# Kernel tuning notes

Hardware: AMD Instinct MI355X
Metric: run time of the kernel (lower is better)

The kernel has to match this reference:

```python
import jax, jax.numpy as jnp
import numpy as np

CAPACITY_FACTOR = 1.25


def setup_inputs() -> dict:
    key = jax.random.key(0)
    k1, k2, k3, k4 = jax.random.split(key, 4)
    B, T, H = 2, 2048, 1024
    E, F = 8, 2048
    x = jax.random.normal(k1, (B, T, H), dtype=jnp.float32)
    Wr = jax.random.normal(k2, (H, E), dtype=jnp.float32) * 0.02
    W1 = jax.random.normal(k3, (E, H, 2 * F), dtype=jnp.float32) * 0.02
    W2 = jax.random.normal(k4, (E, F, H), dtype=jnp.float32) * 0.02
    return {"x": x, "Wr": Wr, "W1": W1, "W2": W2}


def _moe_forward(x, Wr, W1, W2):
    B, T, H = x.shape
    E = Wr.shape[1]
    N = B * T
    cap = max(1, int(CAPACITY_FACTOR * (N * 2 / E)))  # static (shape-derived)

    flat_x = x.reshape(N, H)
    logits = flat_x @ Wr                      # [N, E] (train=False: no noise)
    gate = jax.nn.softmax(logits, axis=-1)
    top2_val, top2_idx = jax.lax.top_k(gate, 2)   # [N,2]

    # --- capacity bookkeeping, matching the torch sequential fill order ---
    e0, e1 = top2_idx[:, 0], top2_idx[:, 1]
    oh0 = jax.nn.one_hot(e0, E, dtype=jnp.int32)  # [N,E]
    oh1 = jax.nn.one_hot(e1, E, dtype=jnp.int32)
    # rank of each token within its expert's k=0 queue (flattened token order)
    pos0 = jnp.take_along_axis(jnp.cumsum(oh0, axis=0), top2_idx[:, :1], axis=1)[:, 0] - 1
    count0 = oh0.sum(axis=0)                      # tokens routed top-1 per expert
    used0 = jnp.minimum(count0, cap)              # slots consumed in k=0 pass
    keep0 = pos0 < cap
    # k=1 pass starts after the slots used by k=0
    pos1 = jnp.take_along_axis(jnp.cumsum(oh1, axis=0), top2_idx[:, 1:2], axis=1)[:, 0] - 1
    pos1 = pos1 + used0[e1]
    keep1 = pos1 < cap

    dummy = E * cap  # drop slot
    slot0 = jnp.where(keep0, e0 * cap + pos0, dummy)
    slot1 = jnp.where(keep1, e1 * cap + pos1, dummy)

    # --- dispatch: [E*cap+1, H] buffer (last row is the drop slot) ---
    buf = jnp.zeros((E * cap + 1, H), dtype=x.dtype)
    buf = buf.at[slot0].set(flat_x).at[slot1].set(flat_x)
    xe = buf[: E * cap].reshape(E, cap, H)

    # --- grouped expert FFN (SwiGLU) ---
    h = jnp.einsum("ech,ehf->ecf", xe, W1)        # [E, cap, 2F]
    a, b = jnp.split(h, 2, axis=-1)
    act = jax.nn.silu(a) * b                      # [E, cap, F]
    out = jnp.einsum("ecf,efh->ech", act, W2)     # [E, cap, H]
    out_flat = out.reshape(E * cap, H)

    # --- combine: gather back per token, weighted by gate values ---
    g0 = out_flat[jnp.where(keep0, slot0, 0)] * keep0[:, None]
    g1 = out_flat[jnp.where(keep1, slot1, 0)] * keep1[:, None]
    y = g0 * top2_val[:, 0:1] + g1 * top2_val[:, 1:2]
    y = y.reshape(B, T, H)

    # --- balance loss ---
    me = 1e-9
    prob_per_expert = gate.mean(axis=0)                 # == mean over (B,T)
    used1 = (oh1 * keep1[:, None].astype(jnp.int32)).sum(axis=0)
    used = (used0 + used1).astype(gate.dtype)
    frac_used = jnp.maximum(used, me) / (N * 2 + me)
    balance_loss = (prob_per_expert * frac_used).sum() * E
    return y, balance_loss


def reference(x, Wr, W1, W2):
    return _moe_forward(x, Wr, W1, W2)
```

## Files before the change

### kernel.cpp

```cpp
#include <hip/hip_runtime.h>
#include <cstdint>

#define E_    8
#define H_    1024
#define F_    2048
#define NTOK  4096
#define CAP   1280
#define ECAP  (E_*CAP)

typedef unsigned short u16;
typedef __attribute__((ext_vector_type(8))) short bf16x8;
typedef __attribute__((ext_vector_type(4))) float f32x4;
typedef __attribute__((ext_vector_type(4))) unsigned short u16x4;

__device__ __forceinline__ u16 f2bf(float f) {
  union { float f; uint32_t u; } v; v.f = f;
  uint32_t r = v.u + 0x7fffu + ((v.u >> 16) & 1u);
  return (u16)(r >> 16);
}

__device__ __forceinline__ void gld16(const void* gsrc, void* ldst) {
  auto g = reinterpret_cast<const __attribute__((address_space(1))) uint32_t*>(
      reinterpret_cast<uintptr_t>(gsrc));
  auto l = reinterpret_cast<__attribute__((address_space(3))) uint32_t*>(
      reinterpret_cast<uintptr_t>(ldst));
  __builtin_amdgcn_global_load_lds(g, l, 16, 0, 0);
}

__device__ __forceinline__ int swz(int row, int chunk) {
  return row * 64 + ((chunk ^ (row & 7)) * 8);
}

__global__ __launch_bounds__(256) void transpose_cvt(const float* __restrict__ in,
                                                     u16* __restrict__ outp,
                                                     int R, int C) {
  __shared__ float tile[64][65];
  size_t base = (size_t)blockIdx.z * R * C;
  int r0 = blockIdx.y * 64, c0 = blockIdx.x * 64;
  int tx = threadIdx.x, ty = threadIdx.y;
#pragma unroll
  for (int i = 0; i < 4; i++) {
    int row = ty + 16 * i;
    float4 v = *(const float4*)(in + base + (size_t)(r0 + row) * C + c0 + tx * 4);
    tile[row][tx * 4 + 0] = v.x;
    tile[row][tx * 4 + 1] = v.y;
    tile[row][tx * 4 + 2] = v.z;
    tile[row][tx * 4 + 3] = v.w;
  }
  __syncthreads();
#pragma unroll
  for (int i = 0; i < 4; i++) {
    int c = ty + 16 * i;
    u16x4 b;
    b.x = f2bf(tile[tx * 4 + 0][c]);
    b.y = f2bf(tile[tx * 4 + 1][c]);
    b.z = f2bf(tile[tx * 4 + 2][c]);
    b.w = f2bf(tile[tx * 4 + 3][c]);
    *(u16x4*)(outp + base + (size_t)(c0 + c) * R + r0 + tx * 4) = b;
  }
}

__global__ __launch_bounds__(256) void router_kernel(const float* __restrict__ x,
                                                     const float* __restrict__ Wr,
                                                     int* __restrict__ e0o, int* __restrict__ e1o,
                                                     float* __restrict__ v0o, float* __restrict__ v1o,
                                                     float* __restrict__ partial) {
  int w = threadIdx.x >> 6, l = threadIdx.x & 63;
  int t = blockIdx.x * 4 + w;
  const float* xr = x + (size_t)t * H_;
  float acc[8] = {0.f,0.f,0.f,0.f,0.f,0.f,0.f,0.f};
#pragma unroll
  for (int it = 0; it < 16; ++it) {
    int h = it * 64 + l;
    float xv = xr[h];
    const float4* wr = (const float4*)(Wr + h * 8);
    float4 wa = wr[0], wb = wr[1];
    acc[0] += xv * wa.x; acc[1] += xv * wa.y; acc[2] += xv * wa.z; acc[3] += xv * wa.w;
    acc[4] += xv * wb.x; acc[5] += xv * wb.y; acc[6] += xv * wb.z; acc[7] += xv * wb.w;
  }
#pragma unroll
  for (int e = 0; e < 8; ++e)
#pragma unroll
    for (int off = 32; off; off >>= 1)
      acc[e] += __shfl_xor(acc[e], off);

  __shared__ float pg[4][8];
  if (l == 0) {
    float mx = acc[0];
#pragma unroll
    for (int e = 1; e < 8; ++e) mx = fmaxf(mx, acc[e]);
    float g[8], s = 0.f;
#pragma unroll
    for (int e = 0; e < 8; ++e) { g[e] = __expf(acc[e] - mx); s += g[e]; }
    float inv = 1.f / s;
#pragma unroll
    for (int e = 0; e < 8; ++e) g[e] *= inv;
    int b0 = 0; float m0 = g[0];
#pragma unroll
    for (int e = 1; e < 8; ++e) if (g[e] > m0) { m0 = g[e]; b0 = e; }
    int b1 = -1; float m1 = -1.f;
#pragma unroll
    for (int e = 0; e < 8; ++e) if (e != b0 && g[e] > m1) { m1 = g[e]; b1 = e; }
    e0o[t] = b0; e1o[t] = b1; v0o[t] = m0; v1o[t] = m1;
#pragma unroll
    for (int e = 0; e < 8; ++e) pg[w][e] = g[e];
  }
  __syncthreads();
  if (threadIdx.x < 8) {
    int e = threadIdx.x;
    partial[blockIdx.x * 8 + e] = pg[0][e] + pg[1][e] + pg[2][e] + pg[3][e];
  }
}

__global__ __launch_bounds__(256) void scan_kernel(const int* __restrict__ e0i, const int* __restrict__ e1i,
                                                   const float* __restrict__ partial,
                                                   int* __restrict__ slot0, int* __restrict__ slot1,
                                                   float* __restrict__ bl_out) {
  __shared__ int c0[256][8], c1[256][8];
  __shared__ float gs[256][8];
  __shared__ int used0_s[8], tot1_s[8];
  int tid = threadIdx.x;

  int le0[16], le1[16];
  int lc0[8] = {0,0,0,0,0,0,0,0}, lc1[8] = {0,0,0,0,0,0,0,0};
  for (int i = 0; i < 16; ++i) {
    int t = tid * 16 + i;
    le0[i] = e0i[t]; le1[i] = e1i[t];
    lc0[le0[i]]++; lc1[le1[i]]++;
  }
#pragma unroll
  for (int e = 0; e < 8; ++e) { c0[tid][e] = lc0[e]; c1[tid][e] = lc1[e]; }

  float g[8] = {0.f,0.f,0.f,0.f,0.f,0.f,0.f,0.f};
  for (int rr = 0; rr < 4; ++rr)
#pragma unroll
    for (int e = 0; e < 8; ++e) g[e] += partial[(tid + rr * 256) * 8 + e];
#pragma unroll
  for (int e = 0; e < 8; ++e) gs[tid][e] = g[e];
  __syncthreads();

  for (int d = 1; d < 256; d <<= 1) {
    int t0[8], t1[8];
    bool a = (tid >= d);
    if (a) {
#pragma unroll
      for (int e = 0; e < 8; ++e) { t0[e] = c0[tid - d][e]; t1[e] = c1[tid - d][e]; }
    }
    __syncthreads();
    if (a) {
#pragma unroll
      for (int e = 0; e < 8; ++e) { c0[tid][e] += t0[e]; c1[tid][e] += t1[e]; }
    }
    __syncthreads();
  }
  for (int s = 128; s > 0; s >>= 1) {
    if (tid < s)
#pragma unroll
      for (int e = 0; e < 8; ++e) gs[tid][e] += gs[tid + s][e];
    __syncthreads();
  }
  if (tid < 8) {
    int e = tid;
    used0_s[e] = min(c0[255][e], CAP);
    tot1_s[e] = c1[255][e];
  }
  __syncthreads();

  int ex0[8], ex1[8];
#pragma unroll
  for (int e = 0; e < 8; ++e) { ex0[e] = c0[tid][e] - lc0[e]; ex1[e] = c1[tid][e] - lc1[e]; }
  int r0c[8] = {0,0,0,0,0,0,0,0}, r1c[8] = {0,0,0,0,0,0,0,0};
  for (int i = 0; i < 16; ++i) {
    int t = tid * 16 + i;
    int e = le0[i];
    int pos = ex0[e] + r0c[e]; r0c[e]++;
    slot0[t] = (pos < CAP) ? (e * CAP + pos) : -1;
    e = le1[i];
    pos = ex1[e] + r1c[e] + used0_s[e]; r1c[e]++;
    slot1[t] = (pos < CAP) ? (e * CAP + pos) : -1;
  }

  if (tid == 0) {
    float bl = 0.f;
    for (int e = 0; e < 8; ++e) {
      int u1 = min(tot1_s[e], max(0, CAP - used0_s[e]));
      float used = (float)(used0_s[e] + u1);
      float fu = fmaxf(used, 1e-9f) / (8192.f + 1e-9f);
      bl += (gs[0][e] / (float)NTOK) * fu;
    }
    bl_out[0] = bl * 8.f;
  }
}

__global__ __launch_bounds__(256) void scatter_kernel(const float* __restrict__ x,
                                                      const int* __restrict__ slot0,
                                                      const int* __restrict__ slot1,
                                                      u16* __restrict__ xe) {
  int t = blockIdx.x, tid = threadIdx.x;
  float4 vv = *(const float4*)(x + (size_t)t * H_ + tid * 4);
  u16x4 b;
  b.x = f2bf(vv.x); b.y = f2bf(vv.y); b.z = f2bf(vv.z); b.w = f2bf(vv.w);
  int s0 = slot0[t], s1 = slot1[t];
  if (s0 >= 0) *(u16x4*)(xe + (size_t)s0 * H_ + tid * 4) = b;
  if (s1 >= 0) *(u16x4*)(xe + (size_t)s1 * H_ + tid * 4) = b;
}

__global__ __launch_bounds__(512, 2) void gemm1_kernel(const u16* __restrict__ xe,
                                                       const u16* __restrict__ W1T,
                                                       u16* __restrict__ act) {
  __shared__ u16 As[2][256 * 64];
  __shared__ u16 Bsa[2][128 * 64];
  __shared__ u16 Bsb[2][128 * 64];

  const int tid = threadIdx.x;
  const int w = tid >> 6, l = tid & 63;
  const int wm = w >> 2, wf = w & 3;

  int bid = blockIdx.x;
  int xcd = bid & 7, idx = bid >> 3;
  int fb = xcd * 2 + idx / 40;
  int mb = idx % 40;
  const int mbase = mb * 256;
  const int nbase = fb * 128;
  const int e = mb / 5;

  const u16* Ap = xe + (size_t)mbase * H_;
  const u16* Ba = W1T + (size_t)e * 4096 * H_ + (size_t)nbase * H_;
  const u16* Bb = Ba + (size_t)F_ * H_;
  const int lrow = l >> 3;
  const int lcol = (((l & 7) ^ lrow) * 8);

  f32x4 acca[8][2] = {};
  f32x4 accb[8][2] = {};

  auto STAGE = [&](int buf, int kt) {
    int k0 = kt * 64;
#pragma unroll
    for (int r = 0; r < 4; ++r) {
      int row0 = w * 32 + r * 8;
      gld16(Ap + (size_t)(row0 + lrow) * H_ + k0 + lcol, &As[buf][row0 * 64]);
    }
#pragma unroll
    for (int r = 0; r < 2; ++r) {
      int row0 = w * 16 + r * 8;
      gld16(Ba + (size_t)(row0 + lrow) * H_ + k0 + lcol, &Bsa[buf][row0 * 64]);
      gld16(Bb + (size_t)(row0 + lrow) * H_ + k0 + lcol, &Bsb[buf][row0 * 64]);
    }
  };

  STAGE(0, 0);
  int cur = 0;

  for (int kt = 0; kt < 16; ++kt) {
    if (kt < 15) {
      STAGE(cur ^ 1, kt + 1);
      asm volatile("s_waitcnt vmcnt(8)" ::: "memory");
    } else {
      asm volatile("s_waitcnt vmcnt(0)" ::: "memory");
    }
    __builtin_amdgcn_s_barrier();

    const u16* Ac = As[cur];
    const u16* Bac = Bsa[cur];
    const u16* Bbc = Bsb[cur];

#pragma unroll
    for (int kk = 0; kk < 2; ++kk) {
      const int ck = kk * 4 + (l >> 4);
      bf16x8 af[8], ba[2], bb[2];
#pragma unroll
      for (int i = 0; i < 8; ++i)
        af[i] = *(const bf16x8*)&Ac[swz(wm * 128 + i * 16 + (l & 15), ck)];
#pragma unroll
      for (int j = 0; j < 2; ++j) {
        ba[j] = *(const bf16x8*)&Bac[swz(wf * 32 + j * 16 + (l & 15), ck)];
        bb[j] = *(const bf16x8*)&Bbc[swz(wf * 32 + j * 16 + (l & 15), ck)];
      }
      asm volatile("s_waitcnt lgkmcnt(0)" ::: "memory");
      __builtin_amdgcn_sched_barrier(0);
      if (kk == 1)
        __builtin_amdgcn_s_barrier();
      __builtin_amdgcn_s_setprio(1);
#pragma unroll
      for (int i = 0; i < 8; ++i)
#pragma unroll
        for (int j = 0; j < 2; ++j) {
          acca[i][j] = __builtin_amdgcn_mfma_f32_16x16x32_bf16(af[i], ba[j], acca[i][j], 0, 0, 0);
          accb[i][j] = __builtin_amdgcn_mfma_f32_16x16x32_bf16(af[i], bb[j], accb[i][j], 0, 0, 0);
        }
      __builtin_amdgcn_s_setprio(0);
    }
    cur ^= 1;
  }

#pragma unroll
  for (int i = 0; i < 8; ++i)
#pragma unroll
    for (int j = 0; j < 2; ++j)
#pragma unroll
      for (int r = 0; r < 4; ++r) {
        int m = mbase + wm * 128 + i * 16 + (l >> 4) * 4 + r;
        int f = nbase + wf * 32 + j * 16 + (l & 15);
        float a = acca[i][j][r];
        float b = accb[i][j][r];
        float s = a / (1.f + __expf(-a));
        act[(size_t)m * F_ + f] = f2bf(s * b);
      }
}

__global__ __launch_bounds__(256, 2) void gemm2_kernel(const u16* __restrict__ act,
                                                       const u16* __restrict__ W2T,
                                                       float* __restrict__ outb) {
  __shared__ u16 As[128 * 64];
  __shared__ u16 Bs[128 * 64];
  const int tid = threadIdx.x;
  const int w = tid >> 6, l = tid & 63;
  const int wm = w & 1, wn = w >> 1;
  const int mbase = blockIdx.y * 128;
  const int nbase = blockIdx.x * 128;
  const int e = mbase / 1280;
  const u16* Ap = act + (size_t)mbase * F_;
  const u16* Bp = W2T + (size_t)e * H_ * F_ + (size_t)nbase * F_;
  const int lrow = l >> 3;
  const int lcol = (((l & 7) ^ lrow) * 8);

  f32x4 acc[4][4] = {};

  for (int kt = 0; kt < 32; ++kt) {
    int k0 = kt * 64;
#pragma unroll
    for (int r = 0; r < 4; ++r) {
      int row0 = w * 32 + r * 8;
      gld16(Ap + (size_t)(row0 + lrow) * F_ + k0 + lcol, &As[row0 * 64]);
      gld16(Bp + (size_t)(row0 + lrow) * F_ + k0 + lcol, &Bs[row0 * 64]);
    }
    __syncthreads();
#pragma unroll
    for (int kk = 0; kk < 64; kk += 32) {
      const int ck = (kk >> 3) + (l >> 4);
      bf16x8 af[4], bf[4];
#pragma unroll
      for (int i = 0; i < 4; ++i)
        af[i] = *(const bf16x8*)&As[swz(wm * 64 + i * 16 + (l & 15), ck)];
#pragma unroll
      for (int j = 0; j < 4; ++j)
        bf[j] = *(const bf16x8*)&Bs[swz(wn * 64 + j * 16 + (l & 15), ck)];
#pragma unroll
      for (int i = 0; i < 4; ++i)
#pragma unroll
        for (int j = 0; j < 4; ++j)
          acc[i][j] = __builtin_amdgcn_mfma_f32_16x16x32_bf16(af[i], bf[j], acc[i][j], 0, 0, 0);
    }
    __syncthreads();
  }
#pragma unroll
  for (int i = 0; i < 4; ++i)
#pragma unroll
    for (int j = 0; j < 4; ++j)
#pragma unroll
      for (int r = 0; r < 4; ++r) {
        int m = mbase + wm * 64 + i * 16 + (l >> 4) * 4 + r;
        int n = nbase + wn * 64 + j * 16 + (l & 15);
        outb[(size_t)m * H_ + n] = acc[i][j][r];
      }
}

__global__ __launch_bounds__(256) void combine_kernel(const float* __restrict__ outb,
                                                      const int* __restrict__ slot0,
                                                      const int* __restrict__ slot1,
                                                      const float* __restrict__ v0,
                                                      const float* __restrict__ v1,
                                                      float* __restrict__ y) {
  int t = blockIdx.x, tid = threadIdx.x;
  int s0 = slot0[t], s1 = slot1[t];
  float w0 = v0[t], w1 = v1[t];
  float4 r; r.x = 0.f; r.y = 0.f; r.z = 0.f; r.w = 0.f;
  if (s0 >= 0) {
    float4 a = *(const float4*)(outb + (size_t)s0 * H_ + tid * 4);
    r.x += w0 * a.x; r.y += w0 * a.y; r.z += w0 * a.z; r.w += w0 * a.w;
  }
  if (s1 >= 0) {
    float4 a = *(const float4*)(outb + (size_t)s1 * H_ + tid * 4);
    r.x += w1 * a.x; r.y += w1 * a.y; r.z += w1 * a.z; r.w += w1 * a.w;
  }
  *(float4*)(y + (size_t)t * H_ + tid * 4) = r;
}

#define OFF_W1T   ((size_t)0)
#define OFF_W2T   ((size_t)67108864)
#define OFF_XE    ((size_t)100663296)
#define OFF_ACT   ((size_t)121634816)
#define OFF_OUTB  ((size_t)163577856)
#define OFF_SLOT0 ((size_t)205520896)
#define OFF_SLOT1 ((size_t)205537280)
#define OFF_V0    ((size_t)205553664)
#define OFF_V1    ((size_t)205570048)
#define OFF_E0    ((size_t)205586432)
#define OFF_E1    ((size_t)205602816)
#define OFF_PART  ((size_t)205619200)

extern "C" void kernel_launch(void* const* d_in, const int* in_sizes, int n_in,
                              void* d_out, int out_size, void* d_ws, size_t ws_size,
                              hipStream_t stream) {
  const float* x  = (const float*)d_in[0];
  const float* Wr = (const float*)d_in[1];
  const float* W1 = (const float*)d_in[2];
  const float* W2 = (const float*)d_in[3];
  float* out = (float*)d_out;

  uint8_t* ws = (uint8_t*)d_ws;
  u16*   W1T   = (u16*)(ws + OFF_W1T);
  u16*   W2T   = (u16*)(ws + OFF_W2T);
  u16*   xe    = (u16*)(ws + OFF_XE);
  u16*   act   = (u16*)(ws + OFF_ACT);
  float* outb  = (float*)(ws + OFF_OUTB);
  int*   slot0 = (int*)(ws + OFF_SLOT0);
  int*   slot1 = (int*)(ws + OFF_SLOT1);
  float* v0    = (float*)(ws + OFF_V0);
  float* v1    = (float*)(ws + OFF_V1);
  int*   e0    = (int*)(ws + OFF_E0);
  int*   e1    = (int*)(ws + OFF_E1);
  float* part  = (float*)(ws + OFF_PART);

  hipMemsetAsync(xe, 0, (size_t)ECAP * H_ * sizeof(u16), stream);

  transpose_cvt<<<dim3(64, 16, 8), dim3(16, 16), 0, stream>>>(W1, W1T, H_, 2 * F_);
  transpose_cvt<<<dim3(16, 32, 8), dim3(16, 16), 0, stream>>>(W2, W2T, F_, H_);

  router_kernel<<<NTOK / 4, 256, 0, stream>>>(x, Wr, e0, e1, v0, v1, part);
  scan_kernel<<<1, 256, 0, stream>>>(e0, e1, part, slot0, slot1, out + (size_t)NTOK * H_);
  scatter_kernel<<<NTOK, 256, 0, stream>>>(x, slot0, slot1, xe);

  gemm1_kernel<<<640, 512, 0, stream>>>(xe, W1T, act);
  gemm2_kernel<<<dim3(H_ / 128, ECAP / 128), 256, 0, stream>>>(act, W2T, outb);

  combine_kernel<<<NTOK, 256, 0, stream>>>(outb, slot0, slot1, v0, v1, out);
}
```

Measured before the change: 256.2 us.

## Split gemm1 K-tiles into half-stages with finer interleaved load/MFMA schedule

Reworks the gemm1 main loop so each 64-wide K tile is staged as two 32-wide halves with a new pair-row swizzle for LDS. The schedule now alternates LDS fragment loads and MFMA bursts for the gate and up projections separately, reusing one B register set. It issues the next half-stage global-to-LDS copy between the halves. The intent is finer overlap of memory traffic with MFMA work and lower register pressure, at the cost of many more workgroup barriers. The fixed vmcnt waits near the loop tail may also not be sufficient.

```diff
diff --git a/kernel.cpp b/kernel.cpp
--- a/kernel.cpp
+++ b/kernel.cpp
@@ -29,6 +29,12 @@
 
 __device__ __forceinline__ int swz(int row, int chunk) {
   return row * 64 + ((chunk ^ (row & 7)) * 8);
+}
+
+__device__ __forceinline__ int swz2(int m, int kc) {
+  int R = m >> 1;
+  int Cl = ((m & 1) << 2) | kc;
+  return R * 64 + ((Cl ^ (R & 7)) << 3);
 }
 
 __global__ __launch_bounds__(256) void transpose_cvt(const float* __restrict__ in,
@@ -208,9 +214,9 @@
 __global__ __launch_bounds__(512, 2) void gemm1_kernel(const u16* __restrict__ xe,
                                                        const u16* __restrict__ W1T,
                                                        u16* __restrict__ act) {
-  __shared__ u16 As[2][256 * 64];
-  __shared__ u16 Bsa[2][128 * 64];
-  __shared__ u16 Bsb[2][128 * 64];
+  __shared__ u16 As[2][2][8192];
+  __shared__ u16 Bsa[2][2][4096];
+  __shared__ u16 Bsb[2][2][4096];
 
   const int tid = threadIdx.x;
   const int w = tid >> 6, l = tid & 63;
@@ -227,71 +233,106 @@
   const u16* Ap = xe + (size_t)mbase * H_;
   const u16* Ba = W1T + (size_t)e * 4096 * H_ + (size_t)nbase * H_;
   const u16* Bb = Ba + (size_t)F_ * H_;
-  const int lrow = l >> 3;
-  const int lcol = (((l & 7) ^ lrow) * 8);
 
   f32x4 acca[8][2] = {};
   f32x4 accb[8][2] = {};
 
-  auto STAGE = [&](int buf, int kt) {
-    int k0 = kt * 64;
-#pragma unroll
-    for (int r = 0; r < 4; ++r) {
-      int row0 = w * 32 + r * 8;
-      gld16(Ap + (size_t)(row0 + lrow) * H_ + k0 + lcol, &As[buf][row0 * 64]);
-    }
+  auto STAGE_H = [&](int buf, int kh, int kt) {
+    const int k0 = kt * 64 + kh * 32;
 #pragma unroll
     for (int r = 0; r < 2; ++r) {
-      int row0 = w * 16 + r * 8;
-      gld16(Ba + (size_t)(row0 + lrow) * H_ + k0 + lcol, &Bsa[buf][row0 * 64]);
-      gld16(Bb + (size_t)(row0 + lrow) * H_ + k0 + lcol, &Bsb[buf][row0 * 64]);
-    }
-  };
-
-  STAGE(0, 0);
-  int cur = 0;
-
-  for (int kt = 0; kt < 16; ++kt) {
-    if (kt < 15) {
-      STAGE(cur ^ 1, kt + 1);
-      asm volatile("s_waitcnt vmcnt(8)" ::: "memory");
-    } else {
-      asm volatile("s_waitcnt vmcnt(0)" ::: "memory");
-    }
-    __builtin_amdgcn_s_barrier();
-
-    const u16* Ac = As[cur];
-    const u16* Bac = Bsa[cur];
-    const u16* Bbc = Bsb[cur];
-
-#pragma unroll
-    for (int kk = 0; kk < 2; ++kk) {
-      const int ck = kk * 4 + (l >> 4);
-      bf16x8 af[8], ba[2], bb[2];
-#pragma unroll
-      for (int i = 0; i < 8; ++i)
-        af[i] = *(const bf16x8*)&Ac[swz(wm * 128 + i * 16 + (l & 15), ck)];
-#pragma unroll
-      for (int j = 0; j < 2; ++j) {
-        ba[j] = *(const bf16x8*)&Bac[swz(wf * 32 + j * 16 + (l & 15), ck)];
-        bb[j] = *(const bf16x8*)&Bbc[swz(wf * 32 + j * 16 + (l & 15), ck)];
-      }
-      asm volatile("s_waitcnt lgkmcnt(0)" ::: "memory");
-      __builtin_amdgcn_sched_barrier(0);
-      if (kk == 1)
-        __builtin_amdgcn_s_barrier();
-      __builtin_amdgcn_s_setprio(1);
-#pragma unroll
-      for (int i = 0; i < 8; ++i)
-#pragma unroll
-        for (int j = 0; j < 2; ++j) {
-          acca[i][j] = __builtin_amdgcn_mfma_f32_16x16x32_bf16(af[i], ba[j], acca[i][j], 0, 0, 0);
-          accb[i][j] = __builtin_amdgcn_mfma_f32_16x16x32_bf16(af[i], bb[j], accb[i][j], 0, 0, 0);
-        }
-      __builtin_amdgcn_s_setprio(0);
-    }
-    cur ^= 1;
-  }
+      int batch = w * 2 + r;
+      int R = batch * 8 + (l >> 3);
+      int Cl = (l & 7) ^ (R & 7);
+      int m = (R << 1) | (Cl >> 2);
+      int kc = Cl & 3;
+      gld16(Ap + (size_t)m * H_ + k0 + kc * 8, &As[buf][kh][batch * 512]);
+    }
+    {
+      int R = w * 8 + (l >> 3);
+      int Cl = (l & 7) ^ (R & 7);
+      int fr = (R << 1) | (Cl >> 2);
+      int kc = Cl & 3;
+      gld16(Ba + (size_t)fr * H_ + k0 + kc * 8, &Bsa[buf][kh][w * 512]);
+    }
+    {
+      int R = w * 8 + (l >> 3);
+      int Cl = (l & 7) ^ (R & 7);
+      int fr = (R << 1) | (Cl >> 2);
+      int kc = Cl & 3;
+      gld16(Bb + (size_t)fr * H_ + k0 + kc * 8, &Bsb[buf][kh][w * 512]);
+    }
+  };
+
+  bf16x8 af[8], bq[2];
+  const int lm = l & 15, lq = l >> 4;
+
+  auto LOAD_A = [&](int buf, int kh) {
+#pragma unroll
+    for (int i = 0; i < 8; ++i)
+      af[i] = *(const bf16x8*)&As[buf][kh][swz2(wm * 128 + i * 16 + lm, lq)];
+  };
+  auto LOAD_BA = [&](int buf, int kh) {
+#pragma unroll
+    for (int j = 0; j < 2; ++j)
+      bq[j] = *(const bf16x8*)&Bsa[buf][kh][swz2(wf * 32 + j * 16 + lm, lq)];
+  };
+  auto LOAD_BB = [&](int buf, int kh) {
+#pragma unroll
+    for (int j = 0; j < 2; ++j)
+      bq[j] = *(const bf16x8*)&Bsb[buf][kh][swz2(wf * 32 + j * 16 + lm, lq)];
+  };
+  auto MFMA_A = [&]() {
+    __builtin_amdgcn_s_setprio(1);
+#pragma unroll
+    for (int i = 0; i < 8; ++i)
+#pragma unroll
+      for (int j = 0; j < 2; ++j)
+        acca[i][j] = __builtin_amdgcn_mfma_f32_16x16x32_bf16(af[i], bq[j], acca[i][j], 0, 0, 0);
+    __builtin_amdgcn_s_setprio(0);
+  };
+  auto MFMA_B = [&]() {
+    __builtin_amdgcn_s_setprio(1);
+#pragma unroll
+    for (int i = 0; i < 8; ++i)
+#pragma unroll
+      for (int j = 0; j < 2; ++j)
+        accb[i][j] = __builtin_amdgcn_mfma_f32_16x16x32_bf16(af[i], bq[j], accb[i][j], 0, 0, 0);
+    __builtin_amdgcn_s_setprio(0);
+  };
+
+#define VMCNT8  asm volatile("s_waitcnt vmcnt(8)" ::: "memory")
+#define LGKM0   do { asm volatile("s_waitcnt lgkmcnt(0)" ::: "memory"); \
+                     __builtin_amdgcn_sched_barrier(0); } while (0)
+#define BAR     __builtin_amdgcn_s_barrier()
+
+  STAGE_H(0, 0, 0);
+  STAGE_H(0, 1, 0);
+  STAGE_H(1, 0, 1);
+
+  auto GROUP = [&](int kt, int c) {
+    if (kt + 1 < 16) STAGE_H(c ^ 1, 1, kt + 1);
+    VMCNT8; BAR;
+    LOAD_A(c, 0); LOAD_BA(c, 0);
+    BAR; LGKM0; MFMA_A(); BAR;
+    LOAD_BB(c, 0);
+    BAR; LGKM0; MFMA_B(); BAR;
+    if (kt + 2 < 16) STAGE_H(c, 0, kt + 2);
+    VMCNT8; BAR;
+    LOAD_A(c, 1); LOAD_BA(c, 1);
+    BAR; LGKM0; MFMA_A(); BAR;
+    LOAD_BB(c, 1);
+    BAR; LGKM0; MFMA_B(); BAR;
+  };
+
+  for (int it = 0; it < 8; ++it) {
+    GROUP(it * 2, 0);
+    GROUP(it * 2 + 1, 1);
+  }
+
+#undef VMCNT8
+#undef LGKM0
+#undef BAR
 
 #pragma unroll
   for (int i = 0; i < 8; ++i)
```

After: 266.6 us. 4.1% more time.
